# Kernel tuning notes

Measured on AMD Instinct MI355X. Metric: run time of the kernel, lower is better.

## Reference

```python
import jax, jax.numpy as jnp
import numpy as np

HIDDEN = 1024
NUM_HEADS = 16
HEAD_DIM = HIDDEN // NUM_HEADS
EPS = 1e-05


def setup_inputs() -> dict:
    key = jax.random.key(0)
    ks = jax.random.split(key, 6)
    B, S = 4, 2048
    x = jax.random.normal(ks[0], (B, S, HIDDEN), dtype=jnp.float32)
    # trunc_normal_(std=0.02) approximated by scaled normal
    w_in = jax.random.normal(ks[1], (3 * HIDDEN, HIDDEN), dtype=jnp.float32) * 0.02
    b_in = jax.random.normal(ks[2], (3 * HIDDEN,), dtype=jnp.float32) * 0.02
    w_norm = jnp.ones((HIDDEN,), dtype=jnp.float32)
    lim = 1.0 / np.sqrt(HIDDEN)
    w_out = jax.random.uniform(ks[3], (HIDDEN, HIDDEN), dtype=jnp.float32, minval=-lim, maxval=lim)
    b_out = jax.random.uniform(ks[4], (HIDDEN,), dtype=jnp.float32, minval=-lim, maxval=lim)
    return {"x": x, "w_in": w_in, "b_in": b_in, "w_norm": w_norm, "w_out": w_out, "b_out": b_out}


def _rms_norm(x, w, eps):
    var = jnp.mean(jnp.square(x), axis=-1, keepdims=True)
    return x * jax.lax.rsqrt(var + eps) * w


def reference(x, w_in, b_in, w_norm, w_out, b_out):
    B, S, _ = x.shape
    xn = _rms_norm(x, w_norm, EPS)
    qkv = jnp.einsum('bsd,ed->bse', xn, w_in) + b_in  # [B,S,3*HIDDEN]
    q, k, v = jnp.split(qkv, 3, axis=-1)
    # [B,S,H*D] -> [B,H,S,D]
    def split_heads(t):
        return t.reshape(B, S, NUM_HEADS, HEAD_DIM).transpose(0, 2, 1, 3)
    q, k, v = split_heads(q), split_heads(k), split_heads(v)
    scale = 1.0 / np.sqrt(HEAD_DIM)
    scores = jnp.einsum('bhqd,bhkd->bhqk', q, k) * scale
    attn = jax.nn.softmax(scores, axis=-1)
    o = jnp.einsum('bhqk,bhkd->bhqd', attn, v)
    o = o.transpose(0, 2, 1, 3).reshape(B, S, HIDDEN)
    return jnp.einsum('bsd,ed->bse', o, w_out) + b_out
```

## Files before the change

kernel.cpp:

```cpp
#include <hip/hip_runtime.h>
#include <stdint.h>

typedef short bf16x4 __attribute__((ext_vector_type(4)));
typedef short bf16x8 __attribute__((ext_vector_type(8)));
typedef _Float16 f16x8 __attribute__((ext_vector_type(8)));
typedef float f32x4 __attribute__((ext_vector_type(4)));
typedef float f32x16 __attribute__((ext_vector_type(16)));
typedef unsigned int u32x4 __attribute__((ext_vector_type(4)));
typedef unsigned int u32x2 __attribute__((ext_vector_type(2)));

#if __has_builtin(__builtin_amdgcn_exp2f)
#define EXP2 __builtin_amdgcn_exp2f
#else
#define EXP2 exp2f
#endif

__device__ __forceinline__ short f2bf(float f) {
  union { float f; uint32_t u; } v; v.f = f;
  uint32_t r = (v.u + 0x7fffu + ((v.u >> 16) & 1u)) >> 16;
  return (short)(uint16_t)r;
}

__device__ __forceinline__ unsigned cvtpk_bf16(float lo, float hi) {
  unsigned r;
  asm("v_cvt_pk_bf16_f32 %0, %1, %2" : "=v"(r) : "v"(lo), "v"(hi));
  return r;
}

#if __has_builtin(__builtin_amdgcn_permlane32_swap)
__device__ __forceinline__ void plane32_swap(unsigned& a, unsigned& b) {
  u32x2 r = __builtin_amdgcn_permlane32_swap(a, b, false, false);
  a = r[0]; b = r[1];
}
__device__ __forceinline__ float xhalf_max(float x) {
  unsigned xu = __builtin_bit_cast(unsigned, x);
  u32x2 r = __builtin_amdgcn_permlane32_swap(xu, xu, false, false);
  return fmaxf(__builtin_bit_cast(float, r[0]), __builtin_bit_cast(float, r[1]));
}
__device__ __forceinline__ float xhalf_sum(float x) {
  unsigned xu = __builtin_bit_cast(unsigned, x);
  u32x2 r = __builtin_amdgcn_permlane32_swap(xu, xu, false, false);
  return __builtin_bit_cast(float, r[0]) + __builtin_bit_cast(float, r[1]);
}
#else
__device__ __forceinline__ void plane32_swap(unsigned& a, unsigned& b) {
  asm("s_nop 1\n\tv_permlane32_swap_b32 %0, %1" : "+v"(a), "+v"(b));
}
__device__ __forceinline__ float xhalf_max(float x) { return fmaxf(x, __shfl_xor(x, 32, 64)); }
__device__ __forceinline__ float xhalf_sum(float x) { return x + __shfl_xor(x, 32, 64); }
#endif

__device__ __forceinline__ float fmax3(float a, float b, float c) {
  return fmaxf(fmaxf(a, b), c);
}

__device__ __forceinline__ float tmax16(const f32x16& s) {
  float a0 = fmax3(s[0], s[1], s[2]);
  float a1 = fmax3(s[3], s[4], s[5]);
  float a2 = fmax3(s[6], s[7], s[8]);
  float a3 = fmax3(s[9], s[10], s[11]);
  float a4 = fmax3(s[12], s[13], s[14]);
  float b0 = fmax3(a0, a1, s[15]);
  float b1 = fmax3(a2, a3, a4);
  return fmaxf(b0, b1);
}
__device__ __forceinline__ float tsum16(const f32x16& s) {
  float a0 = (s[0] + s[1]) + (s[2] + s[3]);
  float a1 = (s[4] + s[5]) + (s[6] + s[7]);
  float a2 = (s[8] + s[9]) + (s[10] + s[11]);
  float a3 = (s[12] + s[13]) + (s[14] + s[15]);
  return (a0 + a1) + (a2 + a3);
}

__device__ __forceinline__ f32x16 zero16() {
  f32x16 z;
#pragma unroll
  for (int i = 0; i < 16; ++i) z[i] = 0.f;
  return z;
}

__device__ __forceinline__ void gld_lds16(const void* g, void* l) {
  __builtin_amdgcn_global_load_lds(
      (__attribute__((address_space(1))) const void*)g,
      (__attribute__((address_space(3))) void*)l, 16, 0, 0);
}

__global__ __launch_bounds__(256) void k_rmsnorm(const float* __restrict__ x,
                                                 const float* __restrict__ wn,
                                                 short* __restrict__ xn) {
  const int row = blockIdx.x;
  const int t = threadIdx.x;
  const float4 v = reinterpret_cast<const float4*>(x + (size_t)row * 1024)[t];
  float ss = v.x * v.x + v.y * v.y + v.z * v.z + v.w * v.w;
#pragma unroll
  for (int m = 32; m >= 1; m >>= 1) ss += __shfl_xor(ss, m, 64);
  __shared__ float red[4];
  if ((t & 63) == 0) red[t >> 6] = ss;
  __syncthreads();
  const float tot = red[0] + red[1] + red[2] + red[3];
  const float rr = rsqrtf(tot * (1.0f / 1024.0f) + 1e-5f);
  const float4 g = reinterpret_cast<const float4*>(wn)[t];
  bf16x4 o;
  o[0] = f2bf(v.x * rr * g.x);
  o[1] = f2bf(v.y * rr * g.y);
  o[2] = f2bf(v.z * rr * g.z);
  o[3] = f2bf(v.w * rr * g.w);
  reinterpret_cast<bf16x4*>(xn + (size_t)row * 1024)[t] = o;
}

__global__ __launch_bounds__(256) void k_cast_bf(const float* __restrict__ in,
                                                 short* __restrict__ out, int n4) {
  int i = blockIdx.x * 256 + threadIdx.x;
  if (i >= n4) return;
  float4 v = reinterpret_cast<const float4*>(in)[i];
  bf16x4 o;
  o[0] = f2bf(v.x); o[1] = f2bf(v.y); o[2] = f2bf(v.z); o[3] = f2bf(v.w);
  reinterpret_cast<bf16x4*>(out)[i] = o;
}

__global__ __launch_bounds__(256) void k_cast_f16(const float* __restrict__ in,
                                                  _Float16* __restrict__ out, int n4) {
  int i = blockIdx.x * 256 + threadIdx.x;
  if (i >= n4) return;
  float4 v = reinterpret_cast<const float4*>(in)[i];
  _Float16 o[4] = {(_Float16)v.x, (_Float16)v.y, (_Float16)v.z, (_Float16)v.w};
  reinterpret_cast<ulong1*>(out)[i] = *reinterpret_cast<ulong1*>(o);
}

__global__ __launch_bounds__(256) void k_gemm_qkv(const short* __restrict__ A,
                                                  const short* __restrict__ B,
                                                  const float* __restrict__ bias,
                                                  short* __restrict__ qb,
                                                  short* __restrict__ kfrag,
                                                  short* __restrict__ vfrag) {
  __shared__ __align__(16) short As[128 * 32];
  __shared__ __align__(16) short Bs[128 * 32];
  const int t = threadIdx.x;
  const int orig = blockIdx.y * 24 + blockIdx.x;
  const int swz = (orig & 7) * 192 + (orig >> 3);
  const long bn0 = (long)(swz % 24) * 128;
  const long bm0 = (long)(swz / 24) * 128;
  const int w = t >> 6, l = t & 63;
  const int wr = (w >> 1) * 64, wc = (w & 1) * 64;
  const int lm = l & 15, h = l >> 4;
  f32x4 acc[4][4];
#pragma unroll
  for (int i = 0; i < 4; ++i)
#pragma unroll
    for (int j = 0; j < 4; ++j) acc[i][j] = (f32x4){0.f, 0.f, 0.f, 0.f};
  const int srow = t >> 2, scol = (t & 3) * 8;
  const short* Ag = A + (bm0 + srow) * 1024 + scol;
  const short* Bg = B + (bn0 + srow) * 1024 + scol;
  short* AsP = As + t * 8;
  short* BsP = Bs + t * 8;
  for (int kt = 0; kt < 32; ++kt) {
    const int k0 = kt << 5;
    gld_lds16(Ag + k0, AsP);
    gld_lds16(Ag + k0 + 64 * 1024, AsP + 2048);
    gld_lds16(Bg + k0, BsP);
    gld_lds16(Bg + k0 + 64 * 1024, BsP + 2048);
    __syncthreads();
    bf16x8 af[4], bfr[4];
#pragma unroll
    for (int mi = 0; mi < 4; ++mi)
      af[mi] = *reinterpret_cast<const bf16x8*>(As + (wr + mi * 16 + lm) * 32 + h * 8);
#pragma unroll
    for (int ni = 0; ni < 4; ++ni)
      bfr[ni] = *reinterpret_cast<const bf16x8*>(Bs + (wc + ni * 16 + lm) * 32 + h * 8);
    __builtin_amdgcn_s_setprio(1);
#pragma unroll
    for (int mi = 0; mi < 4; ++mi)
#pragma unroll
      for (int ni = 0; ni < 4; ++ni)
        acc[mi][ni] = __builtin_amdgcn_mfma_f32_16x16x32_bf16(af[mi], bfr[ni], acc[mi][ni], 0, 0, 0);
    __builtin_amdgcn_s_setprio(0);
    __syncthreads();
  }
#pragma unroll
  for (int ni = 0; ni < 4; ++ni) {
    const int ncol = (int)bn0 + wc + ni * 16 + lm;
    const float bv = bias[ncol];
    const int which = ncol >> 10;
    const int e = ncol & 1023;
    const int hd = e >> 6, d = e & 63;
#pragma unroll
    for (int mi = 0; mi < 4; ++mi) {
#pragma unroll
      for (int r = 0; r < 4; ++r) {
        const long mrow = bm0 + wr + mi * 16 + h * 4 + r;
        const float val = acc[mi][ni][r] + bv;
        const long bh = (mrow >> 11) * 16 + hd;
        const int seq = (int)(mrow & 2047);
        if (which == 0) {
          const long off = (bh * 2048 + seq) * 64 + d;
          qb[off] = f2bf(val * 0.18033688011112042f);
        } else if (which == 1) {
          const long off = ((bh * 64 + (seq >> 5)) * 4 + (d >> 4)) * 512 +
                           ((seq & 31) | (((d >> 3) & 1) << 5)) * 8 + (d & 7);
          kfrag[off] = f2bf(val);
        } else {
          const long off = (((bh * 64 + (seq >> 5)) * 2 + (d >> 5)) * 2 +
                            ((seq >> 4) & 1)) * 512 +
                           ((d & 31) | (((seq >> 3) & 1) << 5)) * 8 + (seq & 7);
          vfrag[off] = f2bf(val);
        }
      }
    }
  }
}

__global__ __launch_bounds__(256) void k_gemm_out(const _Float16* __restrict__ A,
                                                  const _Float16* __restrict__ B,
                                                  const float* __restrict__ bias,
                                                  float* __restrict__ outp) {
  __shared__ __align__(16) _Float16 As[128 * 32];
  __shared__ __align__(16) _Float16 Bs[128 * 32];
  const int t = threadIdx.x;
  const int orig = blockIdx.y * 8 + blockIdx.x;
  const int swz = (orig & 7) * 64 + (orig >> 3);
  const long bn0 = (long)(swz % 8) * 128;
  const long bm0 = (long)(swz / 8) * 128;
  const int w = t >> 6, l = t & 63;
  const int wr = (w >> 1) * 64, wc = (w & 1) * 64;
  const int lm = l & 15, h = l >> 4;
  f32x4 acc[4][4];
#pragma unroll
  for (int i = 0; i < 4; ++i)
#pragma unroll
    for (int j = 0; j < 4; ++j) acc[i][j] = (f32x4){0.f, 0.f, 0.f, 0.f};
  const int srow = t >> 2, scol = (t & 3) * 8;
  const _Float16* Ag = A + (bm0 + srow) * 1024 + scol;
  const _Float16* Bg = B + (bn0 + srow) * 1024 + scol;
  _Float16* AsP = As + t * 8;
  _Float16* BsP = Bs + t * 8;
  for (int kt = 0; kt < 32; ++kt) {
    const int k0 = kt << 5;
    gld_lds16(Ag + k0, AsP);
    gld_lds16(Ag + k0 + 64 * 1024, AsP + 2048);
    gld_lds16(Bg + k0, BsP);
    gld_lds16(Bg + k0 + 64 * 1024, BsP + 2048);
    __syncthreads();
    f16x8 af[4], bfr[4];
#pragma unroll
    for (int mi = 0; mi < 4; ++mi)
      af[mi] = *reinterpret_cast<const f16x8*>(As + (wr + mi * 16 + lm) * 32 + h * 8);
#pragma unroll
    for (int ni = 0; ni < 4; ++ni)
      bfr[ni] = *reinterpret_cast<const f16x8*>(Bs + (wc + ni * 16 + lm) * 32 + h * 8);
    __builtin_amdgcn_s_setprio(1);
#pragma unroll
    for (int mi = 0; mi < 4; ++mi)
#pragma unroll
      for (int ni = 0; ni < 4; ++ni)
        acc[mi][ni] = __builtin_amdgcn_mfma_f32_16x16x32_f16(af[mi], bfr[ni], acc[mi][ni], 0, 0, 0);
    __builtin_amdgcn_s_setprio(0);
    __syncthreads();
  }
#pragma unroll
  for (int ni = 0; ni < 4; ++ni) {
    const int ncol = (int)bn0 + wc + ni * 16 + lm;
    const float bv = bias[ncol];
#pragma unroll
    for (int mi = 0; mi < 4; ++mi) {
#pragma unroll
      for (int r = 0; r < 4; ++r) {
        const long mrow = bm0 + wr + mi * 16 + h * 4 + r;
        outp[mrow * 1024 + ncol] = acc[mi][ni][r] + bv;
      }
    }
  }
}

__global__ __launch_bounds__(256, 4) void k_attn(const short* __restrict__ q,
                                                 const short* __restrict__ kfrag,
                                                 const short* __restrict__ vfrag,
                                                 _Float16* __restrict__ o) {
  const int orig = blockIdx.y * 16 + blockIdx.x;
  const int work = (orig & 7) * 128 + (orig >> 3);
  const int bh = work >> 4;
  const int qt = work & 15;
  const int t = threadIdx.x;
  const int w = t >> 6, l = t & 63;
  const int lq = l & 31, hh = l >> 5;
  const int qrow = qt * 128 + w * 32 + lq;

  bf16x8 qf[4];
  const short* qp = q + ((size_t)(bh * 2048 + qrow)) * 64 + hh * 8;
#pragma unroll
  for (int db = 0; db < 4; ++db)
    qf[db] = *reinterpret_cast<const bf16x8*>(qp + db * 16);

  const short* kfb = kfrag + (size_t)bh * 64 * 2048 + l * 8;
  const short* vfb = vfrag + (size_t)bh * 64 * 2048 + l * 8;

  f32x16 oa0 = zero16(), oa1 = zero16();
  float mr = -1e30f, lr = 0.f;

  auto LOADK = [&](bf16x8* kf, int kt) {
    const short* kp = kfb + (size_t)kt * 2048;
#pragma unroll
    for (int db = 0; db < 4; ++db)
      kf[db] = *reinterpret_cast<const bf16x8*>(kp + db * 512);
  };
  auto LOADV = [&](bf16x8* vf, int kt) {
    const short* vp = vfb + (size_t)kt * 2048;
#pragma unroll
    for (int i = 0; i < 4; ++i)
      vf[i] = *reinterpret_cast<const bf16x8*>(vp + i * 512);
  };

  auto COMPUTE = [&](const bf16x8* kf, const bf16x8* vf) {
    f32x16 s = zero16();
    __builtin_amdgcn_s_setprio(1);
#pragma unroll
    for (int db = 0; db < 4; ++db)
      s = __builtin_amdgcn_mfma_f32_32x32x16_bf16(kf[db], qf[db], s, 0, 0, 0);
    __builtin_amdgcn_s_setprio(0);
    float tm = xhalf_max(tmax16(s));
    if (!__all(tm <= mr + 8.f)) {
      const float mn = fmaxf(mr, tm);
      const float c = EXP2(mr - mn);
      lr *= c;
#pragma unroll
      for (int r = 0; r < 16; ++r) { oa0[r] *= c; oa1[r] *= c; }
      mr = mn;
    }
#pragma unroll
    for (int r = 0; r < 16; ++r) s[r] = EXP2(s[r] - mr);
    lr += tsum16(s);
    __builtin_amdgcn_s_setprio(1);
#pragma unroll
    for (int kg = 0; kg < 2; ++kg) {
      const int b0 = kg * 8;
      unsigned w0 = cvtpk_bf16(s[b0 + 0], s[b0 + 1]);
      unsigned w1 = cvtpk_bf16(s[b0 + 2], s[b0 + 3]);
      unsigned w2 = cvtpk_bf16(s[b0 + 4], s[b0 + 5]);
      unsigned w3 = cvtpk_bf16(s[b0 + 6], s[b0 + 7]);
      plane32_swap(w0, w2);
      plane32_swap(w1, w3);
      u32x4 pw = {w0, w1, w2, w3};
      bf16x8 pf = *reinterpret_cast<bf16x8*>(&pw);
      oa0 = __builtin_amdgcn_mfma_f32_32x32x16_bf16(vf[0 * 2 + kg], pf, oa0, 0, 0, 0);
      oa1 = __builtin_amdgcn_mfma_f32_32x32x16_bf16(vf[1 * 2 + kg], pf, oa1, 0, 0, 0);
    }
    __builtin_amdgcn_s_setprio(0);
  };

  bf16x8 kfA[4], kfB[4], vf[4];
  LOADK(kfA, 0);
  for (int kt = 0; kt < 64; kt += 2) {
    LOADK(kfB, kt + 1);
    LOADV(vf, kt);
    COMPUTE(kfA, vf);
    int k2 = kt + 2; if (k2 > 63) k2 = 63;
    LOADK(kfA, k2);
    LOADV(vf, kt + 1);
    COMPUTE(kfB, vf);
  }
  const float inv = 1.0f / xhalf_sum(lr);
  const int b = bh >> 4, hd = bh & 15;
  _Float16* ob = o + ((size_t)(b * 2048 + qrow)) * 1024 + hd * 64;
#pragma unroll
  for (int r2 = 0; r2 < 16; ++r2) {
    const int d0 = (r2 & 3) + 8 * (r2 >> 2) + 4 * hh;
    ob[d0] = (_Float16)(oa0[r2] * inv);
    ob[d0 + 32] = (_Float16)(oa1[r2] * inv);
  }
}

extern "C" void kernel_launch(void* const* d_in, const int* in_sizes, int n_in,
                              void* d_out, int out_size, void* d_ws, size_t ws_size,
                              hipStream_t stream) {
  const float* x = (const float*)d_in[0];
  const float* w_in = (const float*)d_in[1];
  const float* b_in = (const float*)d_in[2];
  const float* w_norm = (const float*)d_in[3];
  const float* w_out = (const float*)d_in[4];
  const float* b_out = (const float*)d_in[5];
  float* out = (float*)d_out;
  char* ws = (char*)d_ws;
  short* xn = (short*)(ws);
  short* win_b = (short*)(ws + 16777216);
  _Float16* wout_h = (_Float16*)(ws + 23068672);
  short* qb = (short*)(ws + 25165824);
  short* kfrag = (short*)(ws + 41943040);
  short* vfrag = (short*)(ws + 58720256);
  _Float16* ob = (_Float16*)(ws + 75497472);

  k_cast_bf<<<3072, 256, 0, stream>>>(w_in, win_b, 786432);
  k_cast_f16<<<1024, 256, 0, stream>>>(w_out, wout_h, 262144);
  k_rmsnorm<<<8192, 256, 0, stream>>>(x, w_norm, xn);
  k_gemm_qkv<<<dim3(24, 64), 256, 0, stream>>>(xn, win_b, b_in, qb, kfrag, vfrag);
  k_attn<<<dim3(16, 64), 256, 0, stream>>>(qb, kfrag, vfrag, ob);
  k_gemm_out<<<dim3(8, 64), 256, 0, stream>>>(ob, wout_h, b_out, out);
}
```

Baseline: 226.8 us.

## Rewrite QKV GEMM as 256x256 tile, 8-wave, double-buffered pipelined kernel

The QKV projection GEMM moves from 128x128 tiles with 4 waves and a single LDS buffer to 256x256 tiles with 8 waves. K-steps of 64 are double-buffered in XOR-swizzled LDS, and global-to-LDS loads for later steps are interleaved with MFMA phases under fine-grained barriers and vmcnt waits. This is meant to hide load latency, raise data reuse per tile, and cut LDS bank conflicts. In exchange it uses more LDS and registers per block, and the grid shrinks to 384 blocks, which could underfill the GPU.

Result: slower. 250.1 us (+10.3%).

```diff
diff --git a/kernel.cpp b/kernel.cpp
--- a/kernel.cpp
+++ b/kernel.cpp
@@ -127,73 +127,137 @@
   reinterpret_cast<ulong1*>(out)[i] = *reinterpret_cast<ulong1*>(o);
 }
 
-__global__ __launch_bounds__(256) void k_gemm_qkv(const short* __restrict__ A,
-                                                  const short* __restrict__ B,
-                                                  const float* __restrict__ bias,
-                                                  short* __restrict__ qb,
-                                                  short* __restrict__ kfrag,
-                                                  short* __restrict__ vfrag) {
-  __shared__ __align__(16) short As[128 * 32];
-  __shared__ __align__(16) short Bs[128 * 32];
+__global__ __launch_bounds__(512, 2) void k_gemm_qkv(const short* __restrict__ A,
+                                                     const short* __restrict__ B,
+                                                     const float* __restrict__ bias,
+                                                     short* __restrict__ qb,
+                                                     short* __restrict__ kfrag,
+                                                     short* __restrict__ vfrag) {
+  __shared__ __align__(16) short LA[2][2][8192];
+  __shared__ __align__(16) short LB[2][2][8192];
   const int t = threadIdx.x;
-  const int orig = blockIdx.y * 24 + blockIdx.x;
-  const int swz = (orig & 7) * 192 + (orig >> 3);
-  const long bn0 = (long)(swz % 24) * 128;
-  const long bm0 = (long)(swz / 24) * 128;
   const int w = t >> 6, l = t & 63;
-  const int wr = (w >> 1) * 64, wc = (w & 1) * 64;
-  const int lm = l & 15, h = l >> 4;
-  f32x4 acc[4][4];
-#pragma unroll
-  for (int i = 0; i < 4; ++i)
+  const int lm = l & 15, h = l >> 4, sw = lm & 7;
+  const int orig = blockIdx.y * 12 + blockIdx.x;
+  const int swzb = (orig & 7) * 48 + (orig >> 3);
+  const long bn0 = (long)(swzb % 12) * 256;
+  const long bm0 = (long)(swzb / 12) * 256;
+  const int wAh = w >> 2;
+  const int wBh = (w & 3) >> 1;
+  const int nb = (w & 1) * 64;
+  const int g0 = t, g1 = 512 + t;
+  const int r0 = g0 >> 3, r1 = g1 >> 3;
+  const int st0 = r0 * 1024 + ((g0 & 7) ^ (r0 & 7)) * 8;
+  const int st1 = r1 * 1024 + ((g1 & 7) ^ (r1 & 7)) * 8;
+
+  auto STAGE_A = [&](int buf, int half, int kt) {
+    const short* base = A + (bm0 + half * 128) * 1024 + kt * 64;
+    gld_lds16(base + st0, &LA[buf][half][g0 * 8]);
+    gld_lds16(base + st1, &LA[buf][half][g1 * 8]);
+  };
+  auto STAGE_B = [&](int buf, int half, int kt) {
+    const short* base = B + (bn0 + half * 128) * 1024 + kt * 64;
+    gld_lds16(base + st0, &LB[buf][half][g0 * 8]);
+    gld_lds16(base + st1, &LB[buf][half][g1 * 8]);
+  };
+  auto RD_A = [&](int buf, int mi, int ks) {
+    const int row = mi * 16 + lm;
+    return *reinterpret_cast<const bf16x8*>(
+        &LA[buf][wAh][row * 64 + (((ks << 2) + h) ^ sw) * 8]);
+  };
+  auto RD_B = [&](int buf, int ni, int ks) {
+    const int row = nb + ni * 16 + lm;
+    return *reinterpret_cast<const bf16x8*>(
+        &LB[buf][wBh][row * 64 + (((ks << 2) + h) ^ sw) * 8]);
+  };
+
+  f32x4 acc[8][4];
+#pragma unroll
+  for (int i = 0; i < 8; ++i)
 #pragma unroll
     for (int j = 0; j < 4; ++j) acc[i][j] = (f32x4){0.f, 0.f, 0.f, 0.f};
-  const int srow = t >> 2, scol = (t & 3) * 8;
-  const short* Ag = A + (bm0 + srow) * 1024 + scol;
-  const short* Bg = B + (bn0 + srow) * 1024 + scol;
-  short* AsP = As + t * 8;
-  short* BsP = Bs + t * 8;
-  for (int kt = 0; kt < 32; ++kt) {
-    const int k0 = kt << 5;
-    gld_lds16(Ag + k0, AsP);
-    gld_lds16(Ag + k0 + 64 * 1024, AsP + 2048);
-    gld_lds16(Bg + k0, BsP);
-    gld_lds16(Bg + k0 + 64 * 1024, BsP + 2048);
-    __syncthreads();
-    bf16x8 af[4], bfr[4];
+
+  STAGE_B(0, 0, 0); STAGE_B(0, 1, 0);
+  STAGE_A(0, 0, 0); STAGE_A(0, 1, 0);
+  STAGE_B(1, 0, 1); STAGE_A(1, 0, 1);
+  asm volatile("s_waitcnt vmcnt(0)" ::: "memory");
+  __builtin_amdgcn_s_barrier();
+
+  bf16x8 af[4][2], bf0[4], bf1[4];
+  auto MF = [&](bf16x8 (&afr)[4][2], bf16x8 (&bfr)[4], int ks, int mg) {
+    __builtin_amdgcn_s_setprio(1);
 #pragma unroll
     for (int mi = 0; mi < 4; ++mi)
-      af[mi] = *reinterpret_cast<const bf16x8*>(As + (wr + mi * 16 + lm) * 32 + h * 8);
-#pragma unroll
-    for (int ni = 0; ni < 4; ++ni)
-      bfr[ni] = *reinterpret_cast<const bf16x8*>(Bs + (wc + ni * 16 + lm) * 32 + h * 8);
-    __builtin_amdgcn_s_setprio(1);
-#pragma unroll
-    for (int mi = 0; mi < 4; ++mi)
 #pragma unroll
       for (int ni = 0; ni < 4; ++ni)
-        acc[mi][ni] = __builtin_amdgcn_mfma_f32_16x16x32_bf16(af[mi], bfr[ni], acc[mi][ni], 0, 0, 0);
+        acc[mg + mi][ni] = __builtin_amdgcn_mfma_f32_16x16x32_bf16(
+            afr[mi][ks], bfr[ni], acc[mg + mi][ni], 0, 0, 0);
     __builtin_amdgcn_s_setprio(0);
-    __syncthreads();
-  }
+  };
+#define QBAR __builtin_amdgcn_s_barrier()
+#define QLGKM asm volatile("s_waitcnt lgkmcnt(0)" ::: "memory")
+#define QVM4 asm volatile("s_waitcnt vmcnt(4)" ::: "memory")
+
+  for (int i = 0; i < 8; ++i) {
+    const int t2 = 2 * i;
+    const int c1 = (t2 + 1 > 15) ? 15 : t2 + 1;
+    const int c2 = (t2 + 2 > 15) ? 15 : t2 + 2;
+    const int c3 = (t2 + 3 > 15) ? 15 : t2 + 3;
+#pragma unroll
+    for (int mi = 0; mi < 4; ++mi) { af[mi][0] = RD_A(0, mi, 0); af[mi][1] = RD_A(0, mi, 1); }
+#pragma unroll
+    for (int ni = 0; ni < 4; ++ni) bf0[ni] = RD_B(0, ni, 0);
+    STAGE_B(1, 1, c1);
+    QBAR; QLGKM; MF(af, bf0, 0, 0); QBAR;
+#pragma unroll
+    for (int ni = 0; ni < 4; ++ni) bf1[ni] = RD_B(0, ni, 1);
+    STAGE_A(1, 1, c1);
+    QBAR; QLGKM; MF(af, bf1, 1, 0); QBAR;
+#pragma unroll
+    for (int mi = 0; mi < 4; ++mi) { af[mi][0] = RD_A(0, mi + 4, 0); af[mi][1] = RD_A(0, mi + 4, 1); }
+    STAGE_B(0, 0, c2);
+    QBAR; QLGKM; MF(af, bf0, 0, 4); QBAR;
+    STAGE_B(0, 1, c2);
+    QVM4;
+    QBAR; QLGKM; MF(af, bf1, 1, 4); QBAR;
+#pragma unroll
+    for (int mi = 0; mi < 4; ++mi) { af[mi][0] = RD_A(1, mi, 0); af[mi][1] = RD_A(1, mi, 1); }
+#pragma unroll
+    for (int ni = 0; ni < 4; ++ni) bf0[ni] = RD_B(1, ni, 0);
+    STAGE_A(0, 0, c2);
+    QBAR; QLGKM; MF(af, bf0, 0, 0); QBAR;
+#pragma unroll
+    for (int ni = 0; ni < 4; ++ni) bf1[ni] = RD_B(1, ni, 1);
+    STAGE_A(0, 1, c2);
+    QBAR; QLGKM; MF(af, bf1, 1, 0); QBAR;
+#pragma unroll
+    for (int mi = 0; mi < 4; ++mi) { af[mi][0] = RD_A(1, mi + 4, 0); af[mi][1] = RD_A(1, mi + 4, 1); }
+    STAGE_B(1, 0, c3);
+    QBAR; QLGKM; MF(af, bf0, 0, 4); QBAR;
+    STAGE_A(1, 0, c3);
+    QVM4;
+    QBAR; QLGKM; MF(af, bf1, 1, 4); QBAR;
+  }
+
+  const int which = (int)(bn0 >> 10);
+  const long mbase = bm0 + (long)(w >> 2) * 128;
+  const int colbase = (int)bn0 + (w & 3) * 64;
 #pragma unroll
   for (int ni = 0; ni < 4; ++ni) {
-    const int ncol = (int)bn0 + wc + ni * 16 + lm;
+    const int ncol = colbase + ni * 16 + lm;
     const float bv = bias[ncol];
-    const int which = ncol >> 10;
     const int e = ncol & 1023;
     const int hd = e >> 6, d = e & 63;
 #pragma unroll
-    for (int mi = 0; mi < 4; ++mi) {
+    for (int mi = 0; mi < 8; ++mi) {
 #pragma unroll
       for (int r = 0; r < 4; ++r) {
-        const long mrow = bm0 + wr + mi * 16 + h * 4 + r;
+        const long mrow = mbase + mi * 16 + h * 4 + r;
         const float val = acc[mi][ni][r] + bv;
         const long bh = (mrow >> 11) * 16 + hd;
         const int seq = (int)(mrow & 2047);
         if (which == 0) {
-          const long off = (bh * 2048 + seq) * 64 + d;
-          qb[off] = f2bf(val * 0.18033688011112042f);
+          qb[(bh * 2048 + seq) * 64 + d] = f2bf(val * 0.18033688011112042f);
         } else if (which == 1) {
           const long off = ((bh * 64 + (seq >> 5)) * 4 + (d >> 4)) * 512 +
                            ((seq & 31) | (((d >> 3) & 1) << 5)) * 8 + (d & 7);
@@ -390,7 +454,7 @@
   k_cast_bf<<<3072, 256, 0, stream>>>(w_in, win_b, 786432);
   k_cast_f16<<<1024, 256, 0, stream>>>(w_out, wout_h, 262144);
   k_rmsnorm<<<8192, 256, 0, stream>>>(x, w_norm, xn);
-  k_gemm_qkv<<<dim3(24, 64), 256, 0, stream>>>(xn, win_b, b_in, qb, kfrag, vfrag);
+  k_gemm_qkv<<<dim3(12, 32), 512, 0, stream>>>(xn, win_b, b_in, qb, kfrag, vfrag);
   k_attn<<<dim3(16, 64), 256, 0, stream>>>(qb, kfrag, vfrag, ob);
   k_gemm_out<<<dim3(8, 64), 256, 0, stream>>>(ob, wout_h, b_out, out);
 }
```
